# Performance work log

Measured on AMD Instinct MI355X. Metric: run time of the kernel, lower is better.

Reference implementation:

```python
import math
import jax, jax.numpy as jnp
import numpy as np

B, C, T, H, FC, L, K, S, O = 4, 512, 2048, 8, 2048, 6, 3, 256, 1
DK = C // H


def _conv1x1(x, w, b):
    # x: (B,Cin,T), w: (Cout,Cin)
    return jnp.einsum('oc,bct->bot', w, x) + b[None, :, None]


def _conv1d(x, w, b, pad):
    # x: (B,Cin,T), w: (Cout,Cin,K), pad: (left,right)
    y = jax.lax.conv_general_dilated(x, w, (1,), [pad],
                                     dimension_numbers=('NCH', 'OIH', 'NCH'))
    return y + b[None, :, None]


def _layernorm_c(x, g, b, eps=1e-5):
    # LayerNorm over channel dim (module transposes to put channels last)
    m = jnp.mean(x, axis=1, keepdims=True)
    v = jnp.mean((x - m) ** 2, axis=1, keepdims=True)
    return (x - m) * jax.lax.rsqrt(v + eps) * g[None, :, None] + b[None, :, None]


def _attention(x, qw, qb, kw, kb, vw, vb, ow, ob, tri):
    b_, c, t = x.shape
    # reshape(b, H, dk, t).transpose(2,3) -> (B,H,T,dk)
    q = _conv1x1(x, qw, qb).reshape(b_, H, DK, t).transpose(0, 1, 3, 2)
    k = _conv1x1(x, kw, kb).reshape(b_, H, DK, t).transpose(0, 1, 3, 2)
    v = _conv1x1(x, vw, vb).reshape(b_, H, DK, t).transpose(0, 1, 3, 2)
    scores = jnp.einsum('bhtd,bhsd->bhts', q, k) / math.sqrt(DK)
    scores = jnp.where(tri, scores, -1e4)  # causal mask, matches Tensor.where(mask, s, -10000)
    p = jax.nn.softmax(scores, axis=-1)
    o = jnp.einsum('bhts,bhsd->bhtd', p, v)
    o = o.transpose(0, 1, 3, 2).reshape(b_, c, t)
    return _conv1x1(o, ow, ob)


def _ffn(x, x_mask, w1, b1, w2, b2):
    # causal FFN: left pad K-1, activation=None -> relu, p_dropout=0
    y = _conv1d(x * x_mask, w1, b1, (K - 1, 0))
    y = jax.nn.relu(y)
    return _conv1d(y * x_mask, w2, b2, (K - 1, 0)) * x_mask


def _forward(x, norm_f0, x_mask, spk_emb,
             prenet_w, prenet_b, f0pre_w, f0pre_b, cond_w, cond_b, proj_w, proj_b,
             qw, qb, kw, kb, vw, vb, ow, ob,
             ln0_g, ln0_b, ln1_g, ln1_b,
             ffn1_w, ffn1_b, ffn2_w, ffn2_b):
    x = jax.lax.stop_gradient(x)  # torch.detach(x)
    x = x + _conv1x1(spk_emb, cond_w, cond_b)
    x = x + _conv1d(norm_f0, f0pre_w, f0pre_b, (1, 1))
    x = _conv1d(x, prenet_w, prenet_b, (1, 1)) * x_mask
    t = x.shape[2]
    tri = jnp.tril(jnp.ones((t, t), dtype=bool))[None, None]  # subsequent_mask
    x = x * x_mask
    for i in range(L):
        y = _attention(x, qw[i], qb[i], kw[i], kb[i], vw[i], vb[i], ow[i], ob[i], tri)
        x = _layernorm_c(x + y, ln0_g[i], ln0_b[i])
        y = _ffn(x, x_mask, ffn1_w[i], ffn1_b[i], ffn2_w[i], ffn2_b[i])
        x = _layernorm_c(x + y, ln1_g[i], ln1_b[i])
    x = x * x_mask
    return _conv1x1(x, proj_w, proj_b) * x_mask


def setup_inputs() -> dict:
    key = jax.random.key(0)
    ks = iter(jax.random.split(key, 40))
    rn = lambda shape, scale: jax.random.normal(next(ks), shape, jnp.float32) * scale
    inp = {
        'x': rn((B, C, T), 1.0),
        'norm_f0': rn((B, 1, T), 1.0),
        'x_mask': jnp.ones((B, 1, T), jnp.float32),
        'spk_emb': rn((B, S, T), 1.0),
        'prenet_w': rn((C, C, K), (C * K) ** -0.5), 'prenet_b': jnp.zeros((C,), jnp.float32),
        'f0pre_w': rn((C, 1, K), K ** -0.5), 'f0pre_b': jnp.zeros((C,), jnp.float32),
        'cond_w': rn((C, S), S ** -0.5), 'cond_b': jnp.zeros((C,), jnp.float32),
        'proj_w': rn((O, C), C ** -0.5), 'proj_b': jnp.zeros((O,), jnp.float32),
        'qw': rn((L, C, C), C ** -0.5), 'qb': jnp.zeros((L, C), jnp.float32),
        'kw': rn((L, C, C), C ** -0.5), 'kb': jnp.zeros((L, C), jnp.float32),
        'vw': rn((L, C, C), C ** -0.5), 'vb': jnp.zeros((L, C), jnp.float32),
        'ow': rn((L, C, C), C ** -0.5), 'ob': jnp.zeros((L, C), jnp.float32),
        'ln0_g': jnp.ones((L, C), jnp.float32), 'ln0_b': jnp.zeros((L, C), jnp.float32),
        'ln1_g': jnp.ones((L, C), jnp.float32), 'ln1_b': jnp.zeros((L, C), jnp.float32),
        'ffn1_w': rn((L, FC, C, K), (C * K) ** -0.5), 'ffn1_b': jnp.zeros((L, FC), jnp.float32),
        'ffn2_w': rn((L, C, FC, K), (FC * K) ** -0.5), 'ffn2_b': jnp.zeros((L, C), jnp.float32),
    }
    return inp


def reference(x, norm_f0, x_mask, spk_emb,
              prenet_w, prenet_b, f0pre_w, f0pre_b, cond_w, cond_b, proj_w, proj_b,
              qw, qb, kw, kb, vw, vb, ow, ob,
              ln0_g, ln0_b, ln1_g, ln1_b,
              ffn1_w, ffn1_b, ffn2_w, ffn2_b):
    return _forward(x, norm_f0, x_mask, spk_emb,
                    prenet_w, prenet_b, f0pre_w, f0pre_b, cond_w, cond_b, proj_w, proj_b,
                    qw, qb, kw, kb, vw, vb, ow, ob,
                    ln0_g, ln0_b, ln1_g, ln1_b,
                    ffn1_w, ffn1_b, ffn2_w, ffn2_b)
```

## Files before the change

### kernel.cpp

```cpp
#include <hip/hip_runtime.h>
#include <cstdint>
#include <cstddef>

#define T_LEN 2048
#define B_SZ 4
#define C_CH 512
#define H_N 8
#define DK_ 64
#define FC_CH 2048
#define L_N 6
#define KW 3
#define S_CH 256

typedef _Float16 h8 __attribute__((ext_vector_type(8)));
typedef _Float16 h4 __attribute__((ext_vector_type(4)));
typedef float floatx4 __attribute__((ext_vector_type(4)));

__global__ __launch_bounds__(256)
void cast_f16(const float* __restrict__ src, _Float16* __restrict__ dst, int n)
{
    int i = blockIdx.x * 256 + threadIdx.x;
    if (i < n) dst[i] = (_Float16)src[i];
}

__global__ __launch_bounds__(256)
void prepack_k3(const float* __restrict__ src, _Float16* __restrict__ dst, int rk)
{
    const int o = blockIdx.x * 256 + threadIdx.x;
    if (o >= rk) return;
    const size_t row = blockIdx.y;
    const int blk = o / 96, rr = o - blk * 96;
    const int k = rr >> 5, cl = rr & 31;
    dst[row * rk + o] = (_Float16)src[row * rk + (size_t)(blk * 32 + cl) * 3 + k];
}

__global__ __launch_bounds__(256)
void prepack_qkv(const float* __restrict__ qw, const float* __restrict__ kw,
                 const float* __restrict__ vw, const float* __restrict__ qb,
                 const float* __restrict__ kb, const float* __restrict__ vb,
                 _Float16* __restrict__ dst, float* __restrict__ bdst)
{
    int i = blockIdx.x * 256 + threadIdx.x;
    const int total = L_N * 1536 * 512;
    if (i < total) {
        int l = i / (1536 * 512);
        int o = i - l * (1536 * 512);
        int m = o >> 9, c = o & 511;
        const float* s = (m < 512) ? qw : ((m < 1024) ? kw : vw);
        dst[i] = (_Float16)s[((size_t)l * 512 + (m & 511)) * 512 + c];
    }
    if (i < L_N * 1536) {
        int l = i / 1536, m = i - l * 1536;
        const float* s = (m < 512) ? qb : ((m < 1024) ? kb : vb);
        bdst[i] = s[l * 512 + (m & 511)];
    }
}

__global__ __launch_bounds__(256)
void transpose_f0(const float* __restrict__ src, _Float16* __restrict__ dst, int Cd,
                  const float* __restrict__ nf0, const float* __restrict__ f0w,
                  const float* __restrict__ f0b, int do_f0)
{
    __shared__ float tile[32][33];
    const int tl = threadIdx.x & 31;
    const int r  = threadIdx.x >> 5;
    const int t00 = blockIdx.x * 32;
    const int c00 = blockIdx.y * 32;
    const int b   = blockIdx.z;
    const float* s0 = src + (size_t)b * Cd * T_LEN;
#pragma unroll
    for (int rr = 0; rr < 4; ++rr) {
        int cl = r + rr * 8;
        tile[cl][tl] = s0[(size_t)(c00 + cl) * T_LEN + t00 + tl];
    }
    __syncthreads();
    _Float16* d0 = dst + (size_t)b * T_LEN * Cd;
    const int cg = c00 + tl;
#pragma unroll
    for (int rr = 0; rr < 4; ++rr) {
        int tlo = r + rr * 8;
        float v = tile[tl][tlo];
        if (do_f0) {
            int tg = t00 + tlo;
            float a = f0b[cg];
#pragma unroll
            for (int k = 0; k < 3; ++k) {
                int gt = tg + k - 1;
                if (gt >= 0 && gt < T_LEN) a += f0w[cg * 3 + k] * nf0[(size_t)b * T_LEN + gt];
            }
            v += a;
        }
        d0[(size_t)(t00 + tlo) * Cd + cg] = (_Float16)v;
    }
}

template<int KK, int OUTMODE, int MT>
__global__ __launch_bounds__(256)
void conv_gemm_mfma(const _Float16* __restrict__ in, const _Float16* __restrict__ Wpk,
                    const float* __restrict__ bias, const _Float16* __restrict__ res,
                    const float* __restrict__ mask, _Float16* __restrict__ out_v,
                    _Float16* __restrict__ out2,
                    int Cin, int out_stride, int pl, int do_relu,
                    int mask_in, int mask_out)
{
    constexpr int CS   = (KK == 3) ? 32 : 64;
    constexpr int NSEC = (KK == 3) ? 3 : 2;
    constexpr int AST  = NSEC * 32 + 8;
    constexpr int HALO = (KK == 3) ? 2 : 0;
    constexpr int RB   = 128 + 2 * HALO;
    constexpr int BST  = CS + 8;
    constexpr int NAH  = NSEC * MT / 64;
    constexpr int SEGW = NSEC * MT / 8;
    constexpr int IM_N = MT / 32;
    constexpr int NTASK = RB * (CS / 16);
    __shared__ _Float16 sA[MT * AST];
    __shared__ _Float16 sB[RB * BST];

    const int tid = threadIdx.x;
    const int lane = tid & 63;
    const int wid = tid >> 6;
    const int wm = wid >> 1, wt = wid & 1;
    const int r = lane & 15, q4 = lane >> 4;
    const int t0 = blockIdx.x * 128;
    const int m0 = blockIdx.y * MT;
    const int b  = blockIdx.z;
    const float* mk = mask + (size_t)b * T_LEN;

    floatx4 acc[IM_N][4];
#pragma unroll
    for (int i = 0; i < IM_N; ++i)
#pragma unroll
        for (int j = 0; j < 4; ++j)
#pragma unroll
            for (int c = 0; c < 4; ++c) acc[i][j][c] = 0.f;

    const int arow = tid & (MT - 1);
    const int ah0  = (tid / MT) * SEGW;
    const _Float16* ap = Wpk + (size_t)(m0 + arow) * Cin * KK + ah0;

    int brw[2], bcc[2];
    bool bex[2], bval[2];
    _Float16 bm[2];
    const _Float16* bq[2];
    h8 areg[NAH], breg0[2][2], breg1[2][2];
#pragma unroll
    for (int t2 = 0; t2 < 2; ++t2) {
        const int id = tid + t2 * 256;
        bex[t2] = (id < NTASK);
        int row, c16;
        if (KK == 3) { row = id % RB; c16 = (id / RB) * 16; }
        else         { row = id >> 2; c16 = (id & 3) * 16; }
        const int gt = t0 + row - HALO;
        bval[t2] = bex[t2] && gt >= 0 && gt < T_LEN;
        brw[t2] = row; bcc[t2] = c16;
        bm[t2] = (_Float16)((bval[t2] && mask_in) ? mk[gt] : 1.f);
        bq[t2] = in + (size_t)b * T_LEN * Cin + (size_t)gt * Cin + c16;
#pragma unroll
        for (int hh = 0; hh < 2; ++hh)
#pragma unroll
            for (int j = 0; j < 8; ++j) {
                breg0[t2][hh][j] = (_Float16)0.f;
                breg1[t2][hh][j] = (_Float16)0.f;
            }
    }
    const int nch = Cin / CS;
#pragma unroll
    for (int j = 0; j < NAH; ++j) areg[j] = *reinterpret_cast<const h8*>(ap + j * 8);
#pragma unroll
    for (int t2 = 0; t2 < 2; ++t2)
        if (bval[t2]) {
            breg0[t2][0] = *reinterpret_cast<const h8*>(bq[t2]);
            breg0[t2][1] = *reinterpret_cast<const h8*>(bq[t2] + 8);
            breg1[t2][0] = *reinterpret_cast<const h8*>(bq[t2] + CS);
            breg1[t2][1] = *reinterpret_cast<const h8*>(bq[t2] + CS + 8);
            bq[t2] += 2 * CS;
        }

    auto run_chunk = [&](h8 (&br)[2][2], int ci) {
        __syncthreads();
#pragma unroll
        for (int j = 0; j < NAH; ++j)
            *reinterpret_cast<h8*>(&sA[arow * AST + ah0 + j * 8]) = areg[j];
#pragma unroll
        for (int t2 = 0; t2 < 2; ++t2)
            if (bex[t2]) {
                *reinterpret_cast<h8*>(&sB[brw[t2] * BST + bcc[t2]]) = br[t2][0] * bm[t2];
                *reinterpret_cast<h8*>(&sB[brw[t2] * BST + bcc[t2] + 8]) = br[t2][1] * bm[t2];
            }
        __syncthreads();
        if (ci + 1 < nch) {
            ap += CS * KK;
#pragma unroll
            for (int j = 0; j < NAH; ++j) areg[j] = *reinterpret_cast<const h8*>(ap + j * 8);
        }
        if (ci + 2 < nch) {
#pragma unroll
            for (int t2 = 0; t2 < 2; ++t2)
                if (bval[t2]) {
                    br[t2][0] = *reinterpret_cast<const h8*>(bq[t2]);
                    br[t2][1] = *reinterpret_cast<const h8*>(bq[t2] + 8);
                    bq[t2] += CS;
                }
        }
#pragma unroll
        for (int sec = 0; sec < NSEC; ++sec) {
            h8 af[IM_N], bf[4];
#pragma unroll
            for (int im = 0; im < IM_N; ++im)
                af[im] = *reinterpret_cast<const h8*>(&sA[(wm * (MT / 2) + im * 16 + r) * AST + sec * 32 + q4 * 8]);
            const int rb0 = (KK == 3) ? (wt * 64 + r + sec - pl + HALO) : (wt * 64 + r);
            const int cb0 = (KK == 3) ? 0 : sec * 32;
#pragma unroll
            for (int jt = 0; jt < 4; ++jt)
                bf[jt] = *reinterpret_cast<const h8*>(&sB[(rb0 + jt * 16) * BST + cb0 + q4 * 8]);
#pragma unroll
            for (int im = 0; im < IM_N; ++im)
#pragma unroll
                for (int jt = 0; jt < 4; ++jt)
                    acc[im][jt] = __builtin_amdgcn_mfma_f32_16x16x32_f16(af[im], bf[jt], acc[im][jt], 0, 0, 0);
        }
    };

    for (int ci = 0; ci < nch; ci += 2) {
        run_chunk(breg0, ci);
        run_chunk(breg1, ci + 1);
    }

#pragma unroll
    for (int im = 0; im < IM_N; ++im) {
        const int mb = m0 + wm * (MT / 2) + im * 16 + q4 * 4;
        const float4 bv = *reinterpret_cast<const float4*>(&bias[mb]);
#pragma unroll
        for (int jt = 0; jt < 4; ++jt) {
            const int t = t0 + wt * 64 + jt * 16 + r;
            float vv[4];
            vv[0] = acc[im][jt][0] + bv.x;
            vv[1] = acc[im][jt][1] + bv.y;
            vv[2] = acc[im][jt][2] + bv.z;
            vv[3] = acc[im][jt][3] + bv.w;
            if (do_relu) {
#pragma unroll
                for (int c = 0; c < 4; ++c) vv[c] = fmaxf(vv[c], 0.f);
            }
            if (mask_out) {
                const float mv = mk[t];
#pragma unroll
                for (int c = 0; c < 4; ++c) vv[c] *= mv;
            }
            if (OUTMODE == 1) {
                const size_t ob = ((size_t)b * T_LEN + t) * out_stride + mb;
                if (res) {
                    const h4 rv = *reinterpret_cast<const h4*>(&res[ob]);
#pragma unroll
                    for (int c = 0; c < 4; ++c) vv[c] += (float)rv[c];
                }
                h4 hv;
#pragma unroll
                for (int c = 0; c < 4; ++c) hv[c] = (_Float16)vv[c];
                *reinterpret_cast<h4*>(&out_v[ob]) = hv;
            } else {
                if (m0 < 1024) {
                    const size_t ob = ((size_t)b * T_LEN + t) * 1024 + mb;
                    h4 hv;
#pragma unroll
                    for (int c = 0; c < 4; ++c) hv[c] = (_Float16)vv[c];
                    *reinterpret_cast<h4*>(&out_v[ob]) = hv;
                } else {
#pragma unroll
                    for (int reg = 0; reg < 4; ++reg)
                        out2[((size_t)b * C_CH + (mb - 1024) + reg) * T_LEN + t] = (_Float16)vv[reg];
                }
            }
        }
    }
}

__global__ __launch_bounds__(256)
void flash_attn_mfma(const _Float16* __restrict__ qk, const _Float16* __restrict__ vt,
                     _Float16* __restrict__ o)
{
    __shared__ _Float16 sK[64 * 72];
    __shared__ _Float16 sVt[64 * 72];
    __shared__ _Float16 sP[64 * 72];
    const int tid = threadIdx.x;
    const int lane = tid & 63;
    const int w = tid >> 6;
    const int r = lane & 15, q4 = lane >> 4;
    const int qt0 = (int)(31 - blockIdx.x) * 64;
    const int h = blockIdx.y, b = blockIdx.z;
    const size_t tb = (size_t)b * T_LEN;
    const int hq = h * 64, hk = 512 + h * 64;
    const _Float16* vbase = vt + ((size_t)b * C_CH + h * 64) * T_LEN;

    h8 qf[2];
#pragma unroll
    for (int dc = 0; dc < 2; ++dc) {
        h8 t = *reinterpret_cast<const h8*>(
            &qk[(tb + qt0 + w * 16 + r) * 1024 + hq + dc * 32 + q4 * 8]);
        qf[dc] = t * (_Float16)0.125f;
    }

    floatx4 oacc[4];
    float mrow = -__builtin_inff();
    float lrow = 0.f;
#pragma unroll
    for (int jd = 0; jd < 4; ++jd)
#pragma unroll
        for (int c = 0; c < 4; ++c) oacc[jd][c] = 0.f;

    const int qg = qt0 + w * 16 + r;
    const int nk = (qt0 >> 6) + 1;
    for (int kt = 0; kt < nk; ++kt) {
        const int kt0 = kt * 64;
        __syncthreads();
        {
            int row = tid >> 2, c16 = (tid & 3) * 16;
            const _Float16* src = &qk[(tb + kt0 + row) * 1024 + hk + c16];
            *reinterpret_cast<h8*>(&sK[row * 72 + c16]) = *reinterpret_cast<const h8*>(src);
            *reinterpret_cast<h8*>(&sK[row * 72 + c16 + 8]) = *reinterpret_cast<const h8*>(src + 8);
        }
#pragma unroll
        for (int p = 0; p < 2; ++p) {
            int id = p * 256 + tid;
            int d = id >> 3, s8 = (id & 7) * 8;
            *reinterpret_cast<h8*>(&sVt[d * 72 + s8]) =
                *reinterpret_cast<const h8*>(&vbase[(size_t)d * T_LEN + kt0 + s8]);
        }
        __syncthreads();

        floatx4 sacc[4];
#pragma unroll
        for (int js = 0; js < 4; ++js)
#pragma unroll
            for (int c = 0; c < 4; ++c) sacc[js][c] = 0.f;
#pragma unroll
        for (int dc = 0; dc < 2; ++dc) {
            h8 kf[4];
#pragma unroll
            for (int js = 0; js < 4; ++js)
                kf[js] = *reinterpret_cast<const h8*>(&sK[(js * 16 + r) * 72 + dc * 32 + q4 * 8]);
#pragma unroll
            for (int js = 0; js < 4; ++js)
                sacc[js] = __builtin_amdgcn_mfma_f32_16x16x32_f16(kf[js], qf[dc], sacc[js], 0, 0, 0);
        }
#pragma unroll
        for (int js = 0; js < 4; ++js) {
            const int sb = kt0 + js * 16 + q4 * 4;
#pragma unroll
            for (int reg = 0; reg < 4; ++reg)
                if (sb + reg > qg) sacc[js][reg] = -1e4f;
        }
        float mt;
        {
            float a = fmaxf(fmaxf(sacc[0][0], sacc[0][1]), fmaxf(sacc[0][2], sacc[0][3]));
            float bm = fmaxf(fmaxf(sacc[1][0], sacc[1][1]), fmaxf(sacc[1][2], sacc[1][3]));
            float c = fmaxf(fmaxf(sacc[2][0], sacc[2][1]), fmaxf(sacc[2][2], sacc[2][3]));
            float d = fmaxf(fmaxf(sacc[3][0], sacc[3][1]), fmaxf(sacc[3][2], sacc[3][3]));
            mt = fmaxf(fmaxf(a, bm), fmaxf(c, d));
        }
        mt = fmaxf(mt, __shfl_xor(mt, 16));
        mt = fmaxf(mt, __shfl_xor(mt, 32));
        const float mn = fmaxf(mrow, mt);
        const float alpha = __expf(mrow - mn);
        mrow = mn;
        float rs = 0.f;
#pragma unroll
        for (int js = 0; js < 4; ++js)
#pragma unroll
            for (int reg = 0; reg < 4; ++reg) {
                float p = __expf(sacc[js][reg] - mn);
                sacc[js][reg] = p;
                rs += p;
            }
        rs += __shfl_xor(rs, 16);
        rs += __shfl_xor(rs, 32);
        lrow = lrow * alpha + rs;
        float ao[4];
#pragma unroll
        for (int reg = 0; reg < 4; ++reg) ao[reg] = __shfl(alpha, (q4 << 2) + reg, 16);
#pragma unroll
        for (int jd = 0; jd < 4; ++jd)
#pragma unroll
            for (int reg = 0; reg < 4; ++reg) oacc[jd][reg] *= ao[reg];
#pragma unroll
        for (int js = 0; js < 4; ++js) {
            h4 hv;
#pragma unroll
            for (int reg = 0; reg < 4; ++reg) hv[reg] = (_Float16)sacc[js][reg];
            *reinterpret_cast<h4*>(&sP[(w * 16 + r) * 72 + js * 16 + q4 * 4]) = hv;
        }
#pragma unroll
        for (int sc = 0; sc < 2; ++sc) {
            h8 pf = *reinterpret_cast<const h8*>(&sP[(w * 16 + r) * 72 + sc * 32 + q4 * 8]);
            h8 vf[4];
#pragma unroll
            for (int jd = 0; jd < 4; ++jd)
                vf[jd] = *reinterpret_cast<const h8*>(&sVt[(jd * 16 + r) * 72 + sc * 32 + q4 * 8]);
#pragma unroll
            for (int jd = 0; jd < 4; ++jd)
                oacc[jd] = __builtin_amdgcn_mfma_f32_16x16x32_f16(pf, vf[jd], oacc[jd], 0, 0, 0);
        }
    }
    const float linv = 1.f / lrow;
    float li[4];
#pragma unroll
    for (int reg = 0; reg < 4; ++reg) li[reg] = __shfl(linv, (q4 << 2) + reg, 16);
#pragma unroll
    for (int reg = 0; reg < 4; ++reg) {
        const size_t rowb = (tb + qt0 + w * 16 + (q4 << 2) + reg) * 512 + h * 64 + r;
#pragma unroll
        for (int jd = 0; jd < 4; ++jd)
            o[rowb + jd * 16] = (_Float16)(oacc[jd][reg] * li[reg]);
    }
}

__global__ __launch_bounds__(256)
void ln_kernel(const _Float16* __restrict__ x, const _Float16* __restrict__ y,
               const float* __restrict__ g, const float* __restrict__ be,
               _Float16* __restrict__ outx)
{
    const int w = threadIdx.x >> 6, lane = threadIdx.x & 63;
    const int t = blockIdx.x * 4 + w, b = blockIdx.y;
    const size_t base = ((size_t)b * T_LEN + t) * C_CH + lane * 8;
    h8 xv = *reinterpret_cast<const h8*>(&x[base]);
    h8 yv = *reinterpret_cast<const h8*>(&y[base]);
    float v[8];
#pragma unroll
    for (int i = 0; i < 8; ++i) v[i] = (float)xv[i] + (float)yv[i];
    float s = 0.f, s2 = 0.f;
#pragma unroll
    for (int i = 0; i < 8; ++i) { s += v[i]; s2 += v[i] * v[i]; }
#pragma unroll
    for (int off = 1; off < 64; off <<= 1) {
        s  += __shfl_xor(s, off);
        s2 += __shfl_xor(s2, off);
    }
    const float mean = s * (1.f / C_CH);
    const float var  = s2 * (1.f / C_CH) - mean * mean;
    const float rstd = rsqrtf(var + 1e-5f);
    float4 g0 = *reinterpret_cast<const float4*>(&g[lane * 8]);
    float4 g1 = *reinterpret_cast<const float4*>(&g[lane * 8 + 4]);
    float4 b0 = *reinterpret_cast<const float4*>(&be[lane * 8]);
    float4 b1 = *reinterpret_cast<const float4*>(&be[lane * 8 + 4]);
    const float gg[8] = {g0.x, g0.y, g0.z, g0.w, g1.x, g1.y, g1.z, g1.w};
    const float bb[8] = {b0.x, b0.y, b0.z, b0.w, b1.x, b1.y, b1.z, b1.w};
    h8 ov;
#pragma unroll
    for (int i = 0; i < 8; ++i)
        ov[i] = (_Float16)((v[i] - mean) * rstd * gg[i] + bb[i]);
    *reinterpret_cast<h8*>(&outx[base]) = ov;
}

__global__ __launch_bounds__(256)
void proj_kernel(const _Float16* __restrict__ x, const float* __restrict__ pw,
                 const float* __restrict__ pb, const float* __restrict__ mask,
                 float* __restrict__ out)
{
    const int w = threadIdx.x >> 6, lane = threadIdx.x & 63;
    const int t = blockIdx.x * 4 + w, b = blockIdx.y;
    const size_t base = ((size_t)b * T_LEN + t) * C_CH + lane * 8;
    h8 xv = *reinterpret_cast<const h8*>(&x[base]);
    float4 p0 = *reinterpret_cast<const float4*>(&pw[lane * 8]);
    float4 p1 = *reinterpret_cast<const float4*>(&pw[lane * 8 + 4]);
    const float pp[8] = {p0.x, p0.y, p0.z, p0.w, p1.x, p1.y, p1.z, p1.w};
    float s = 0.f;
#pragma unroll
    for (int i = 0; i < 8; ++i) s += (float)xv[i] * pp[i];
#pragma unroll
    for (int off = 1; off < 64; off <<= 1) s += __shfl_xor(s, off);
    if (lane == 0) {
        const float mv = mask[(size_t)b * T_LEN + t];
        out[(size_t)b * T_LEN + t] = (s * mv + pb[0]) * mv;
    }
}

extern "C" void kernel_launch(void* const* d_in, const int* in_sizes, int n_in,
                              void* d_out, int out_size, void* d_ws, size_t ws_size,
                              hipStream_t stream)
{
    const float* x    = (const float*)d_in[0];
    const float* nf0  = (const float*)d_in[1];
    const float* xm   = (const float*)d_in[2];
    const float* spk  = (const float*)d_in[3];
    const float* prw  = (const float*)d_in[4];
    const float* prb  = (const float*)d_in[5];
    const float* f0w  = (const float*)d_in[6];
    const float* f0b  = (const float*)d_in[7];
    const float* cw   = (const float*)d_in[8];
    const float* cb   = (const float*)d_in[9];
    const float* pjw  = (const float*)d_in[10];
    const float* pjb  = (const float*)d_in[11];
    const float* qw   = (const float*)d_in[12];
    const float* qb   = (const float*)d_in[13];
    const float* kw   = (const float*)d_in[14];
    const float* kb   = (const float*)d_in[15];
    const float* vw   = (const float*)d_in[16];
    const float* vb   = (const float*)d_in[17];
    const float* ow   = (const float*)d_in[18];
    const float* ob   = (const float*)d_in[19];
    const float* ln0g = (const float*)d_in[20];
    const float* ln0b = (const float*)d_in[21];
    const float* ln1g = (const float*)d_in[22];
    const float* ln1b = (const float*)d_in[23];
    const float* f1w  = (const float*)d_in[24];
    const float* f1b  = (const float*)d_in[25];
    const float* f2w  = (const float*)d_in[26];
    const float* f2b  = (const float*)d_in[27];
    float* out = (float*)d_out;

    const size_t NCT = (size_t)B_SZ * C_CH * T_LEN;
    char* wp = (char*)d_ws;
    _Float16* xbuf = (_Float16*)wp; wp += NCT * 2;
    _Float16* t0h  = (_Float16*)wp; wp += NCT * 2;
    _Float16* qk   = (_Float16*)wp; wp += NCT * 4;
    _Float16* vt   = (_Float16*)wp; wp += NCT * 2;
    _Float16* obf  = (_Float16*)wp; wp += NCT * 2;
    _Float16* h1   = (_Float16*)wp; wp += NCT * 8;
    _Float16* xT   = h1;
    _Float16* spkT = obf;
    _Float16* Wqkv = (_Float16*)wp; wp += (size_t)L_N * 1536 * 512 * 2;
    _Float16* Wo   = (_Float16*)wp; wp += (size_t)L_N * 512 * 512 * 2;
    _Float16* Wcnd = (_Float16*)wp; wp += (size_t)512 * 256 * 2;
    _Float16* Wpre = (_Float16*)wp; wp += (size_t)512 * 512 * 3 * 2;
    _Float16* Wf1  = (_Float16*)wp; wp += (size_t)L_N * 2048 * 512 * 3 * 2;
    _Float16* Wf2  = (_Float16*)wp; wp += (size_t)L_N * 512 * 2048 * 3 * 2;
    float*    Bqkv = (float*)wp;    wp += (size_t)L_N * 1536 * 4;

    dim3 blk(256);
    dim3 gC64(16, 8, B_SZ);
    dim3 gQKV(16, 12, B_SZ);
    dim3 gF(16, 16, B_SZ);
    dim3 gAT(32, H_N, B_SZ);
    dim3 gLN(T_LEN / 4, B_SZ);

    {
        int n;
        n = C_CH * S_CH;       cast_f16<<<(n + 255) / 256, blk, 0, stream>>>(cw, Wcnd, n);
        n = L_N * C_CH * C_CH; cast_f16<<<(n + 255) / 256, blk, 0, stream>>>(ow, Wo, n);
        prepack_k3<<<dim3(6, C_CH), blk, 0, stream>>>(prw, Wpre, C_CH * 3);
        prepack_k3<<<dim3(6, L_N * FC_CH), blk, 0, stream>>>(f1w, Wf1, C_CH * 3);
        prepack_k3<<<dim3(24, L_N * C_CH), blk, 0, stream>>>(f2w, Wf2, FC_CH * 3);
        n = L_N * 1536 * 512;  prepack_qkv<<<(n + 255) / 256, blk, 0, stream>>>(qw, kw, vw, qb, kb, vb, Wqkv, Bqkv);
    }

    transpose_f0<<<dim3(64, 16, B_SZ), blk, 0, stream>>>(x, xT, C_CH, nf0, f0w, f0b, 1);
    transpose_f0<<<dim3(64, 8, B_SZ), blk, 0, stream>>>(spk, spkT, S_CH, nullptr, nullptr, nullptr, 0);
    conv_gemm_mfma<1, 1, 64><<<gC64, blk, 0, stream>>>(spkT, Wcnd, cb, xT, xm, t0h, nullptr, S_CH, C_CH, 0, 0, 0, 0);
    conv_gemm_mfma<3, 1, 64><<<gC64, blk, 0, stream>>>(t0h, Wpre, prb, nullptr, xm, xbuf, nullptr, C_CH, C_CH, 1, 0, 0, 1);

    for (int l = 0; l < L_N; ++l) {
        const size_t bo = (size_t)l * C_CH;
        conv_gemm_mfma<1, 3, 128><<<gQKV, blk, 0, stream>>>(xbuf, Wqkv + (size_t)l * 1536 * 512, Bqkv + l * 1536,
                                                            nullptr, xm, qk, vt, C_CH, 1024, 0, 0, 0, 0);
        flash_attn_mfma<<<gAT, blk, 0, stream>>>(qk, vt, obf);
        conv_gemm_mfma<1, 1, 64><<<gC64, blk, 0, stream>>>(obf, Wo + (size_t)l * 512 * 512, ob + bo,
                                                           nullptr, xm, t0h, nullptr, C_CH, C_CH, 0, 0, 0, 0);
        ln_kernel<<<gLN, blk, 0, stream>>>(xbuf, t0h, ln0g + bo, ln0b + bo, xbuf);
        conv_gemm_mfma<3, 1, 128><<<gF, blk, 0, stream>>>(xbuf, Wf1 + (size_t)l * FC_CH * C_CH * 3, f1b + (size_t)l * FC_CH,
                                                          nullptr, xm, h1, nullptr, C_CH, FC_CH, 2, 1, 1, 0);
        conv_gemm_mfma<3, 1, 64><<<gC64, blk, 0, stream>>>(h1, Wf2 + (size_t)l * C_CH * FC_CH * 3, f2b + bo,
                                                           nullptr, xm, t0h, nullptr, FC_CH, C_CH, 2, 0, 1, 1);
        ln_kernel<<<gLN, blk, 0, stream>>>(xbuf, t0h, ln1g + bo, ln1b + bo, xbuf);
    }
    proj_kernel<<<gLN, blk, 0, stream>>>(xbuf, pjw, pjb, xm, out);
}
```

Measured before the change: 2.178 ms.

## Double-buffer LDS tiles in conv GEMM and shrink M tile for QKV/FFN1

The conv GEMM kernel now keeps two shared-memory buffers for the A and B tiles. It stages the next chunk into the alternate buffer while MFMAs run on the current one, which cuts the barriers per chunk from two to one. The QKV and FFN1 launches also switch from a 128-row to a 64-row M tile and double their grid y dimension, trading weight reuse for more blocks and possibly better occupancy. The doubled LDS footprint may reduce how many blocks fit on a CU.

```diff
diff --git a/kernel.cpp b/kernel.cpp
--- a/kernel.cpp
+++ b/kernel.cpp
@@ -113,8 +113,8 @@
     constexpr int SEGW = NSEC * MT / 8;
     constexpr int IM_N = MT / 32;
     constexpr int NTASK = RB * (CS / 16);
-    __shared__ _Float16 sA[MT * AST];
-    __shared__ _Float16 sB[RB * BST];
+    __shared__ _Float16 sA[2][MT * AST];
+    __shared__ _Float16 sB[2][RB * BST];
 
     const int tid = threadIdx.x;
     const int lane = tid & 63;
@@ -164,6 +164,33 @@
             }
     }
     const int nch = Cin / CS;
+
+    auto loadA = [&]() {
+        ap += CS * KK;
+#pragma unroll
+        for (int j = 0; j < NAH; ++j) areg[j] = *reinterpret_cast<const h8*>(ap + j * 8);
+    };
+    auto loadB = [&](h8 (&br)[2][2]) {
+#pragma unroll
+        for (int t2 = 0; t2 < 2; ++t2)
+            if (bval[t2]) {
+                br[t2][0] = *reinterpret_cast<const h8*>(bq[t2]);
+                br[t2][1] = *reinterpret_cast<const h8*>(bq[t2] + 8);
+                bq[t2] += CS;
+            }
+    };
+    auto stage = [&](int pb, h8 (&br)[2][2]) {
+#pragma unroll
+        for (int j = 0; j < NAH; ++j)
+            *reinterpret_cast<h8*>(&sA[pb][arow * AST + ah0 + j * 8]) = areg[j];
+#pragma unroll
+        for (int t2 = 0; t2 < 2; ++t2)
+            if (bex[t2]) {
+                *reinterpret_cast<h8*>(&sB[pb][brw[t2] * BST + bcc[t2]]) = br[t2][0] * bm[t2];
+                *reinterpret_cast<h8*>(&sB[pb][brw[t2] * BST + bcc[t2] + 8]) = br[t2][1] * bm[t2];
+            }
+    };
+
 #pragma unroll
     for (int j = 0; j < NAH; ++j) areg[j] = *reinterpret_cast<const h8*>(ap + j * 8);
 #pragma unroll
@@ -175,55 +202,53 @@
             breg1[t2][1] = *reinterpret_cast<const h8*>(bq[t2] + CS + 8);
             bq[t2] += 2 * CS;
         }
-
-    auto run_chunk = [&](h8 (&br)[2][2], int ci) {
-        __syncthreads();
-#pragma unroll
-        for (int j = 0; j < NAH; ++j)
-            *reinterpret_cast<h8*>(&sA[arow * AST + ah0 + j * 8]) = areg[j];
-#pragma unroll
-        for (int t2 = 0; t2 < 2; ++t2)
-            if (bex[t2]) {
-                *reinterpret_cast<h8*>(&sB[brw[t2] * BST + bcc[t2]]) = br[t2][0] * bm[t2];
-                *reinterpret_cast<h8*>(&sB[brw[t2] * BST + bcc[t2] + 8]) = br[t2][1] * bm[t2];
-            }
-        __syncthreads();
-        if (ci + 1 < nch) {
-            ap += CS * KK;
-#pragma unroll
-            for (int j = 0; j < NAH; ++j) areg[j] = *reinterpret_cast<const h8*>(ap + j * 8);
-        }
-        if (ci + 2 < nch) {
-#pragma unroll
-            for (int t2 = 0; t2 < 2; ++t2)
-                if (bval[t2]) {
-                    br[t2][0] = *reinterpret_cast<const h8*>(bq[t2]);
-                    br[t2][1] = *reinterpret_cast<const h8*>(bq[t2] + 8);
-                    bq[t2] += CS;
-                }
-        }
-#pragma unroll
-        for (int sec = 0; sec < NSEC; ++sec) {
+    stage(0, breg0);
+    loadA();
+    loadB(breg0);
+    __syncthreads();
+
+    auto body = [&](int pb, int cc, h8 (&br)[2][2]) {
+        h8 af0[IM_N], bf0[4];
+#pragma unroll
+        for (int im = 0; im < IM_N; ++im)
+            af0[im] = *reinterpret_cast<const h8*>(&sA[pb][(wm * (MT / 2) + im * 16 + r) * AST + q4 * 8]);
+        {
+            const int rb0 = (KK == 3) ? (wt * 64 + r - pl + HALO) : (wt * 64 + r);
+#pragma unroll
+            for (int jt = 0; jt < 4; ++jt)
+                bf0[jt] = *reinterpret_cast<const h8*>(&sB[pb][(rb0 + jt * 16) * BST + q4 * 8]);
+        }
+        if (cc + 1 < nch) stage(pb ^ 1, br);
+        if (cc + 2 < nch) loadA();
+        if (cc + 3 < nch) loadB(br);
+#pragma unroll
+        for (int im = 0; im < IM_N; ++im)
+#pragma unroll
+            for (int jt = 0; jt < 4; ++jt)
+                acc[im][jt] = __builtin_amdgcn_mfma_f32_16x16x32_f16(af0[im], bf0[jt], acc[im][jt], 0, 0, 0);
+#pragma unroll
+        for (int sec = 1; sec < NSEC; ++sec) {
             h8 af[IM_N], bf[4];
 #pragma unroll
             for (int im = 0; im < IM_N; ++im)
-                af[im] = *reinterpret_cast<const h8*>(&sA[(wm * (MT / 2) + im * 16 + r) * AST + sec * 32 + q4 * 8]);
+                af[im] = *reinterpret_cast<const h8*>(&sA[pb][(wm * (MT / 2) + im * 16 + r) * AST + sec * 32 + q4 * 8]);
             const int rb0 = (KK == 3) ? (wt * 64 + r + sec - pl + HALO) : (wt * 64 + r);
             const int cb0 = (KK == 3) ? 0 : sec * 32;
 #pragma unroll
             for (int jt = 0; jt < 4; ++jt)
-                bf[jt] = *reinterpret_cast<const h8*>(&sB[(rb0 + jt * 16) * BST + cb0 + q4 * 8]);
+                bf[jt] = *reinterpret_cast<const h8*>(&sB[pb][(rb0 + jt * 16) * BST + cb0 + q4 * 8]);
 #pragma unroll
             for (int im = 0; im < IM_N; ++im)
 #pragma unroll
                 for (int jt = 0; jt < 4; ++jt)
                     acc[im][jt] = __builtin_amdgcn_mfma_f32_16x16x32_f16(af[im], bf[jt], acc[im][jt], 0, 0, 0);
         }
+        __syncthreads();
     };
 
     for (int ci = 0; ci < nch; ci += 2) {
-        run_chunk(breg0, ci);
-        run_chunk(breg1, ci + 1);
+        body(0, ci, breg1);
+        body(1, ci + 1, breg0);
     }
 
 #pragma unroll
@@ -528,8 +553,8 @@
 
     dim3 blk(256);
     dim3 gC64(16, 8, B_SZ);
-    dim3 gQKV(16, 12, B_SZ);
-    dim3 gF(16, 16, B_SZ);
+    dim3 gQKV(16, 24, B_SZ);
+    dim3 gF(16, 32, B_SZ);
     dim3 gAT(32, H_N, B_SZ);
     dim3 gLN(T_LEN / 4, B_SZ);
 
@@ -550,14 +575,14 @@
 
     for (int l = 0; l < L_N; ++l) {
         const size_t bo = (size_t)l * C_CH;
-        conv_gemm_mfma<1, 3, 128><<<gQKV, blk, 0, stream>>>(xbuf, Wqkv + (size_t)l * 1536 * 512, Bqkv + l * 1536,
-                                                            nullptr, xm, qk, vt, C_CH, 1024, 0, 0, 0, 0);
+        conv_gemm_mfma<1, 3, 64><<<gQKV, blk, 0, stream>>>(xbuf, Wqkv + (size_t)l * 1536 * 512, Bqkv + l * 1536,
+                                                           nullptr, xm, qk, vt, C_CH, 1024, 0, 0, 0, 0);
         flash_attn_mfma<<<gAT, blk, 0, stream>>>(qk, vt, obf);
         conv_gemm_mfma<1, 1, 64><<<gC64, blk, 0, stream>>>(obf, Wo + (size_t)l * 512 * 512, ob + bo,
                                                            nullptr, xm, t0h, nullptr, C_CH, C_CH, 0, 0, 0, 0);
         ln_kernel<<<gLN, blk, 0, stream>>>(xbuf, t0h, ln0g + bo, ln0b + bo, xbuf);
-        conv_gemm_mfma<3, 1, 128><<<gF, blk, 0, stream>>>(xbuf, Wf1 + (size_t)l * FC_CH * C_CH * 3, f1b + (size_t)l * FC_CH,
-                                                          nullptr, xm, h1, nullptr, C_CH, FC_CH, 2, 1, 1, 0);
+        conv_gemm_mfma<3, 1, 64><<<gF, blk, 0, stream>>>(xbuf, Wf1 + (size_t)l * FC_CH * C_CH * 3, f1b + (size_t)l * FC_CH,
+                                                         nullptr, xm, h1, nullptr, C_CH, FC_CH, 2, 1, 1, 0);
         conv_gemm_mfma<3, 1, 64><<<gC64, blk, 0, stream>>>(h1, Wf2 + (size_t)l * C_CH * FC_CH * 3, f2b + bo,
                                                            nullptr, xm, t0h, nullptr, FC_CH, C_CH, 2, 0, 1, 1);
         ln_kernel<<<gLN, blk, 0, stream>>>(xbuf, t0h, ln1g + bo, ln1b + bo, xbuf);
```

Result: slower. 2.223 ms (+2.0%).
